# Performance work log

Measured on AMD Instinct MI355X. Metric: run time of the kernel, lower is better.

Reference implementation:

```python
import jax, jax.numpy as jnp
import numpy as np

HEADS = 16
DIM_HEAD = 64
EPS = 1e-8


def setup_inputs() -> dict:
    key = jax.random.key(0)
    ks = jax.random.split(key, 5)
    B, N, D = 2, 2048, 1024
    inner = HEADS * DIM_HEAD
    return {
        "x": jax.random.normal(ks[0], (B, N, D), jnp.float32),
        "Wq": jax.random.normal(ks[1], (D, inner), jnp.float32) * (D ** -0.5),
        "Wkv": jax.random.normal(ks[2], (D, 2 * inner), jnp.float32) * (D ** -0.5),
        "Wo": jax.random.normal(ks[3], (inner, D), jnp.float32) * (inner ** -0.5),
        "bo": jax.random.normal(ks[4], (D,), jnp.float32) * 0.02,
    }


def reference(x, Wq, Wkv, Wo, bo):
    # Self-attention (context = x), causal, memory-efficient path.
    # The chunked online-softmax in the source is mathematically equivalent to:
    #   gm = rowwise max of raw (unmasked) scores (stop-gradient, as in .detach())
    #   p  = exp(s - gm) with causal-masked entries zeroed (exp(-finfo.max) == 0)
    #   out = (p @ v) / (sum_j p + eps)
    B, N, D = x.shape
    H, Dh = HEADS, DIM_HEAD
    scale = Dh ** -0.5

    q = (x @ Wq).reshape(B, N, H, Dh).transpose(0, 2, 1, 3)  # b h n d
    kv = x @ Wkv
    k = kv[..., : H * Dh].reshape(B, N, H, Dh).transpose(0, 2, 1, 3)
    v = kv[..., H * Dh :].reshape(B, N, H, Dh).transpose(0, 2, 1, 3)

    s = jnp.einsum("bhid,bhjd->bhij", q * scale, k)  # b h i j
    gm = jax.lax.stop_gradient(jnp.max(s, axis=-1, keepdims=True))
    causal_mask = jnp.triu(jnp.ones((N, N), bool), 1)  # True above diagonal -> masked
    p = jnp.where(causal_mask, 0.0, jnp.exp(s - gm))
    num = jnp.einsum("bhij,bhjd->bhid", p, v)
    out = num / (jnp.sum(p, axis=-1, keepdims=True) + EPS)  # b h n d

    out = out.transpose(0, 2, 1, 3).reshape(B, N, H * Dh)  # b n (h d)
    return out @ Wo + bo
```

## Files before the change

### kernel.cpp

```cpp
#include <hip/hip_runtime.h>

typedef _Float16 f16;
typedef __attribute__((ext_vector_type(8))) _Float16 f16x8;
typedef __attribute__((ext_vector_type(4))) _Float16 f16x4;
typedef __attribute__((ext_vector_type(4))) float   f32x4;

typedef unsigned int u32;
typedef __attribute__((address_space(1))) const u32 gu32;
typedef __attribute__((address_space(3))) u32 lu32;

__device__ inline void gll16(const void* g, void* l) {
  __builtin_amdgcn_global_load_lds((gu32*)g, (lu32*)l, 16, 0, 0);
}

__global__ void prep(const float* __restrict__ Wq, const float* __restrict__ Wkv,
                     const float* __restrict__ Wo, const float* __restrict__ x,
                     f16* __restrict__ WqkvT, f16* __restrict__ WoT, f16* __restrict__ xb) {
  __shared__ float tile[32][33];
  int z = blockIdx.z;
  int tx = threadIdx.x, ty = threadIdx.y;
  if (z == 3) {
    size_t flat = ((size_t)(blockIdx.y * 64 + blockIdx.x) * 256 + ty * 32 + tx) * 2;
    for (int i = 0; i < 2; i++) {
      float4 v = ((const float4*)x)[flat + i];
      f16x4 r = { (f16)v.x, (f16)v.y, (f16)v.z, (f16)v.w };
      ((f16x4*)xb)[flat + i] = r;
    }
    return;
  }
  const float* src; f16* dst; int W;
  if (z == 0)      { src = Wq;  dst = WqkvT;                       W = 1024; }
  else if (z == 1) { src = Wkv; dst = WqkvT + (size_t)1024 * 1024; W = 2048; }
  else             { src = Wo;  dst = WoT;                         W = 1024; }
  int c0 = blockIdx.x * 32, r0 = blockIdx.y * 32;
  if (c0 >= W) return;
  for (int i = 0; i < 4; i++)
    tile[ty + i * 8][tx] = src[(size_t)(r0 + ty + i * 8) * W + c0 + tx];
  __syncthreads();
  for (int i = 0; i < 4; i++)
    dst[(size_t)(c0 + ty + i * 8) * 1024 + r0 + tx] = (f16)tile[tx][ty + i * 8];
}

__global__ __launch_bounds__(256) void gemm1(
    const f16* __restrict__ A, const f16* __restrict__ Bt,
    f16* __restrict__ qb, f16* __restrict__ kb, f16* __restrict__ vtb) {
  const int K = 1024;
  __shared__ f16 As[2][128 * 32];
  __shared__ f16 Bs[2][128 * 32];
  int tid = threadIdx.x;
  int wave = tid >> 6, lane = tid & 63, quad = lane >> 4, l16 = lane & 15;
  int m0 = blockIdx.y * 128, n0 = blockIdx.x * 128;
  int wr = (wave >> 1) * 64, wc = (wave & 1) * 64;

  f32x4 acc[4][4] = {};

  int gA = (((lane & 3) ^ ((lane >> 3) & 3))) * 8;
  const f16* Ag = A  + (size_t)(m0 + wave * 32 + (lane >> 2)) * K + gA;
  const f16* Bg = Bt + (size_t)(n0 + wave * 32 + (lane >> 2)) * K + gA;
  int rsz = (l16 >> 1) & 3;

  {
    f16* Asw = &As[0][0] + wave * 1024;
    f16* Bsw = &Bs[0][0] + wave * 1024;
    gll16(Ag, Asw);
    gll16(Ag + (size_t)16 * K, Asw + 512);
    gll16(Bg, Bsw);
    gll16(Bg + (size_t)16 * K, Bsw + 512);
  }
  __syncthreads();

  int cur = 0;
  for (int k0 = 0; k0 < K; k0 += 32) {
    if (k0 + 32 < K) {
      f16* Asw = &As[cur ^ 1][0] + wave * 1024;
      f16* Bsw = &Bs[cur ^ 1][0] + wave * 1024;
      gll16(Ag + k0 + 32, Asw);
      gll16(Ag + (size_t)16 * K + k0 + 32, Asw + 512);
      gll16(Bg + k0 + 32, Bsw);
      gll16(Bg + (size_t)16 * K + k0 + 32, Bsw + 512);
    }
    const f16* Asr = &As[cur][0];
    const f16* Bsr = &Bs[cur][0];
    f16x8 af[4], bf[4];
    for (int mt = 0; mt < 4; mt++)
      af[mt] = *(const f16x8*)&Asr[(wr + mt * 16 + l16) * 32 + ((quad ^ rsz) << 3)];
    for (int nt = 0; nt < 4; nt++)
      bf[nt] = *(const f16x8*)&Bsr[(wc + nt * 16 + l16) * 32 + ((quad ^ rsz) << 3)];
    for (int mt = 0; mt < 4; mt++)
      for (int nt = 0; nt < 4; nt++)
        acc[mt][nt] = __builtin_amdgcn_mfma_f32_16x16x32_f16(af[mt], bf[nt], acc[mt][nt], 0, 0, 0);
    __syncthreads();
    cur ^= 1;
  }

  if (n0 < 2048) {
    for (int mt = 0; mt < 4; mt++)
      for (int nt = 0; nt < 4; nt++)
        for (int r = 0; r < 4; r++) {
          int row = m0 + wr + mt * 16 + quad * 4 + r;
          int col = n0 + wc + nt * 16 + l16;
          float v = acc[mt][nt][r];
          int b = row >> 11, n = row & 2047;
          if (col < 1024) {
            qb[(((size_t)b * 16 + (col >> 6)) * 2048 + n) * 64 + (col & 63)] =
                (f16)(v * 0.1803368801111137f);
          } else {
            int c = col - 1024;
            kb[(((size_t)b * 16 + (c >> 6)) * 2048 + n) * 64 + (c & 63)] = (f16)v;
          }
        }
  } else {
    for (int mt = 0; mt < 4; mt++)
      for (int nt = 0; nt < 4; nt++) {
        int rb = m0 + wr + mt * 16 + quad * 4;
        int c  = n0 + wc + nt * 16 + l16 - 2048;
        int b = rb >> 11, n = rb & 2047;
        f16x4 pk = { (f16)acc[mt][nt][0], (f16)acc[mt][nt][1],
                     (f16)acc[mt][nt][2], (f16)acc[mt][nt][3] };
        size_t idx = (((size_t)(b * 16 + (c >> 6)) * 32 + (n >> 6)) * 64 + (c & 63)) * 64 + (n & 63);
        *(f16x4*)&vtb[idx] = pk;
      }
  }
}

__global__ __launch_bounds__(256) void gemm2(
    const f16* __restrict__ A, const f16* __restrict__ Bt,
    const float* __restrict__ bo, float* __restrict__ outf) {
  const int K = 1024;
  __shared__ f16 As[2][128 * 32];
  __shared__ f16 Bs[2][64 * 32];
  int tid = threadIdx.x;
  int wave = tid >> 6, lane = tid & 63, quad = lane >> 4, l16 = lane & 15;
  int m0 = blockIdx.y * 128, n0 = blockIdx.x * 64;
  int wr = (wave >> 1) * 64, wc = (wave & 1) * 32;

  f32x4 acc[4][2] = {};

  int gA = (((lane & 3) ^ ((lane >> 3) & 3))) * 8;
  const f16* Ag = A  + (size_t)(m0 + wave * 32 + (lane >> 2)) * K + gA;
  const f16* Bg = Bt + (size_t)(n0 + wave * 16 + (lane >> 2)) * K + gA;
  int rsz = (l16 >> 1) & 3;

  {
    f16* Asw = &As[0][0] + wave * 1024;
    f16* Bsw = &Bs[0][0] + wave * 512;
    gll16(Ag, Asw);
    gll16(Ag + (size_t)16 * K, Asw + 512);
    gll16(Bg, Bsw);
  }
  __syncthreads();

  int cur = 0;
  for (int k0 = 0; k0 < K; k0 += 32) {
    if (k0 + 32 < K) {
      f16* Asw = &As[cur ^ 1][0] + wave * 1024;
      f16* Bsw = &Bs[cur ^ 1][0] + wave * 512;
      gll16(Ag + k0 + 32, Asw);
      gll16(Ag + (size_t)16 * K + k0 + 32, Asw + 512);
      gll16(Bg + k0 + 32, Bsw);
    }
    const f16* Asr = &As[cur][0];
    const f16* Bsr = &Bs[cur][0];
    f16x8 af[4], bf[2];
    for (int mt = 0; mt < 4; mt++)
      af[mt] = *(const f16x8*)&Asr[(wr + mt * 16 + l16) * 32 + ((quad ^ rsz) << 3)];
    for (int nt = 0; nt < 2; nt++)
      bf[nt] = *(const f16x8*)&Bsr[(wc + nt * 16 + l16) * 32 + ((quad ^ rsz) << 3)];
    for (int mt = 0; mt < 4; mt++)
      for (int nt = 0; nt < 2; nt++)
        acc[mt][nt] = __builtin_amdgcn_mfma_f32_16x16x32_f16(af[mt], bf[nt], acc[mt][nt], 0, 0, 0);
    __syncthreads();
    cur ^= 1;
  }

  for (int mt = 0; mt < 4; mt++)
    for (int nt = 0; nt < 2; nt++)
      for (int r = 0; r < 4; r++) {
        int row = m0 + wr + mt * 16 + quad * 4 + r;
        int col = n0 + wc + nt * 16 + l16;
        outf[(size_t)row * 1024 + col] = acc[mt][nt][r] + bo[col];
      }
}

__global__ __launch_bounds__(256, 4) void attn(
    const f16* __restrict__ qb, const f16* __restrict__ kb,
    const f16* __restrict__ vtb, f16* __restrict__ ob) {
  __shared__ f16 Ks[2][64 * 64];
  __shared__ f16 Vs[2][64 * 64];
  __shared__ f16 Ps[4][16 * 64];
  int tid = threadIdx.x, wave = tid >> 6, lane = tid & 63, quad = lane >> 4, l16 = lane & 15;
  int l7 = l16 & 7;

  int bx = blockIdx.x;
  int q = bx >> 8, r = bx & 255;
  int xcd = r & 7, idx = r >> 3;
  int bh = xcd * 4 + (idx & 3);
  int srem = idx >> 2;
  int t = (q == 0) ? srem : (q == 1) ? 15 - srem : (q == 2) ? 16 + srem : 31 - srem;
  int qi0 = t * 64;
  int b = bh >> 4, h = bh & 15;

  const f16* Q  = qb + (size_t)bh * 2048 * 64;
  const char* Kg = (const char*)(kb + (size_t)bh * 2048 * 64);
  const char* Vbase = (const char*)(vtb + (size_t)bh * 32 * 4096);
  int wq0 = qi0 + wave * 16;
  int i = wq0 + l16;

  f16x8 qf[2];
  for (int ks = 0; ks < 2; ks++)
    qf[ks] = *(const f16x8*)&Q[(size_t)(wq0 + l16) * 64 + ks * 32 + quad * 8];

  f32x4 acc[4] = {};
  float lrow = 0.f;

  int sg = ((lane & 7) ^ ((lane >> 3) & 7)) * 16;
  int jl = wave * 16 + (lane >> 3);

  int end = qi0 + 64;

  gll16(Kg + (size_t)jl * 128 + sg,          (char*)&Ks[0][0] + wave * 2048);
  gll16(Kg + (size_t)(jl + 8) * 128 + sg,    (char*)&Ks[0][0] + wave * 2048 + 1024);
  gll16(Vbase + (size_t)jl * 128 + sg,       (char*)&Vs[0][0] + wave * 2048);
  gll16(Vbase + (size_t)(jl + 8) * 128 + sg, (char*)&Vs[0][0] + wave * 2048 + 1024);
  __syncthreads();

  int cur = 0;
  for (int j0 = 0; j0 < end; j0 += 64) {
    if (j0 + 64 < end) {
      const char* kg = Kg + (size_t)(j0 + 64) * 128;
      const char* vt = Vbase + (size_t)((j0 + 64) >> 6) * 8192;
      char* kd = (char*)&Ks[cur ^ 1][0] + wave * 2048;
      char* vd = (char*)&Vs[cur ^ 1][0] + wave * 2048;
      gll16(kg + (size_t)jl * 128 + sg,       kd);
      gll16(kg + (size_t)(jl + 8) * 128 + sg, kd + 1024);
      gll16(vt + (size_t)jl * 128 + sg,       vd);
      gll16(vt + (size_t)(jl + 8) * 128 + sg, vd + 1024);
    }

    {
      const f16* KsC = &Ks[cur][0];
      const f16* VsC = &Vs[cur][0];
      f16x8 kf[4][2], vf[4][2];
      for (int nt = 0; nt < 4; nt++)
        for (int ks = 0; ks < 2; ks++) {
          int pos = ((ks * 4 + quad) ^ l7) << 3;
          kf[nt][ks] = *(const f16x8*)&KsC[(nt * 16 + l16) * 64 + pos];
          vf[nt][ks] = *(const f16x8*)&VsC[(nt * 16 + l16) * 64 + pos];
        }

      f32x4 st[4];
      for (int nt = 0; nt < 4; nt++) {
        f32x4 z = {0.f, 0.f, 0.f, 0.f};
        z = __builtin_amdgcn_mfma_f32_16x16x32_f16(kf[nt][0], qf[0], z, 0, 0, 0);
        z = __builtin_amdgcn_mfma_f32_16x16x32_f16(kf[nt][1], qf[1], z, 0, 0, 0);
        st[nt] = z;
      }
      if (j0 + 63 > wq0) {
        for (int nt = 0; nt < 4; nt++) {
          int jc = j0 + nt * 16 + quad * 4;
          for (int rr = 0; rr < 4; rr++)
            st[nt][rr] = (jc + rr <= i) ? st[nt][rr] : -1e30f;
        }
      }
      float psum = 0.f;
      for (int nt = 0; nt < 4; nt++) {
        f16x4 pk;
        for (int rr = 0; rr < 4; rr++) {
          float p = __builtin_amdgcn_exp2f(st[nt][rr] - 14.426950408889634f);
          psum += p;
          pk[rr] = (f16)p;
        }
        int pos = (nt * 2 + (quad >> 1)) ^ l7;
        *(f16x4*)((char*)&Ps[wave][0] + l16 * 128 + pos * 16 + (quad & 1) * 8) = pk;
      }
      psum += __shfl_xor(psum, 16);
      psum += __shfl_xor(psum, 32);
      lrow += psum;

      for (int ks = 0; ks < 2; ks++) {
        f16x8 pf = *(const f16x8*)((char*)&Ps[wave][0] + l16 * 128 + (((ks * 4 + quad) ^ l7) * 16));
        for (int nt = 0; nt < 4; nt++)
          acc[nt] = __builtin_amdgcn_mfma_f32_16x16x32_f16(vf[nt][ks], pf, acc[nt], 0, 0, 0);
      }
    }
    __syncthreads();
    cur ^= 1;
  }

  float inv = 1.f / (lrow + 1e-8f);
  int n = wq0 + l16;
  for (int nt = 0; nt < 4; nt++) {
    f16x4 o = { (f16)(acc[nt][0] * inv), (f16)(acc[nt][1] * inv),
                (f16)(acc[nt][2] * inv), (f16)(acc[nt][3] * inv) };
    *(f16x4*)&ob[((size_t)b * 2048 + n) * 1024 + h * 64 + nt * 16 + quad * 4] = o;
  }
}

extern "C" void kernel_launch(void* const* d_in, const int* in_sizes, int n_in,
                              void* d_out, int out_size, void* d_ws, size_t ws_size,
                              hipStream_t stream) {
  const float* x   = (const float*)d_in[0];
  const float* Wq  = (const float*)d_in[1];
  const float* Wkv = (const float*)d_in[2];
  const float* Wo  = (const float*)d_in[3];
  const float* bo  = (const float*)d_in[4];
  float* out = (float*)d_out;

  char* ws = (char*)d_ws;
  f16* xb    = (f16*)ws;  ws += (size_t)4096 * 1024 * 2;
  f16* WqkvT = (f16*)ws;  ws += (size_t)3072 * 1024 * 2;
  f16* WoT   = (f16*)ws;  ws += (size_t)1024 * 1024 * 2;
  f16* qb    = (f16*)ws;  ws += (size_t)32 * 2048 * 64 * 2;
  f16* kb    = (f16*)ws;  ws += (size_t)32 * 2048 * 64 * 2;
  f16* vtb   = (f16*)ws;  ws += (size_t)32 * 64 * 2048 * 2;
  f16* ob    = xb;

  prep<<<dim3(64, 32, 4), dim3(32, 8), 0, stream>>>(Wq, Wkv, Wo, x, WqkvT, WoT, xb);
  gemm1<<<dim3(24, 32), 256, 0, stream>>>(xb, WqkvT, qb, kb, vtb);
  attn<<<dim3(1024), 256, 0, stream>>>(qb, kb, vtb, ob);
  gemm2<<<dim3(16, 32), 256, 0, stream>>>(ob, WoT, bo, out);
}
```

Before: 178.9 us.

## Restructure QKV GEMM into 256x256 tiles with 8 waves and phased MFMA scheduling

Rewrites the QKV projection GEMM to use 256x256 block tiles with 512 threads, K-tiles of 64 with XOR-swizzled LDS, and a two-buffer prefetch issued two tiles ahead. Each K-tile is split into four barrier-separated phases, with s_setprio raised around the MFMA bursts to interleave waves. The aim is more data reuse per LDS byte and better overlap of global loads with matrix math. The cost is that the grid shrinks to 192 blocks, which may underfill the 256 CUs, and that register pressure rises with 32 accumulators per thread.

```diff
diff --git a/kernel.cpp b/kernel.cpp
--- a/kernel.cpp
+++ b/kernel.cpp
@@ -41,60 +41,87 @@
     dst[(size_t)(c0 + ty + i * 8) * 1024 + r0 + tx] = (f16)tile[tx][ty + i * 8];
 }
 
-__global__ __launch_bounds__(256) void gemm1(
+#define G1_PHASE(qq, SA, SB, FIRST)                                          \
+  {                                                                          \
+    if (FIRST) {                                                             \
+      _Pragma("unroll") for (int nt = 0; nt < 4; nt++)                       \
+        _Pragma("unroll") for (int ks = 0; ks < 2; ks++)                     \
+          bf[nt][ks] = *(const f16x8*)&SB[(wc + nt * 16 + l16) * 64 +        \
+                                          (((ks * 4 + quad) ^ l7) << 3)];    \
+    }                                                                        \
+    _Pragma("unroll") for (int j = 0; j < 2; j++)                            \
+      _Pragma("unroll") for (int ks = 0; ks < 2; ks++)                       \
+        af[j][ks] = *(const f16x8*)&SA[(wr + (2 * (qq) + j) * 16 + l16) * 64 \
+                                       + (((ks * 4 + quad) ^ l7) << 3)];     \
+    __builtin_amdgcn_s_barrier();                                            \
+    asm volatile("s_waitcnt lgkmcnt(0)" ::: "memory");                       \
+    __builtin_amdgcn_s_setprio(1);                                           \
+    _Pragma("unroll") for (int j = 0; j < 2; j++)                            \
+      _Pragma("unroll") for (int nt = 0; nt < 4; nt++) {                     \
+        acc[2 * (qq) + j][nt] = __builtin_amdgcn_mfma_f32_16x16x32_f16(      \
+            af[j][0], bf[nt][0], acc[2 * (qq) + j][nt], 0, 0, 0);            \
+        acc[2 * (qq) + j][nt] = __builtin_amdgcn_mfma_f32_16x16x32_f16(      \
+            af[j][1], bf[nt][1], acc[2 * (qq) + j][nt], 0, 0, 0);            \
+      }                                                                      \
+    __builtin_amdgcn_s_setprio(0);                                           \
+  }
+
+#define G1_STAGE(ktile, SA, SB)                                              \
+  { int kk = (ktile) * 64;                                                   \
+    _Pragma("unroll") for (int i2 = 0; i2 < 4; i2++) {                       \
+      gll16(Ag0 + (size_t)(i2 * 64) * 1024 + kk,                             \
+            (char*)(SA) + i2 * 8192 + wave * 1024);                          \
+      gll16(Bg0 + (size_t)(i2 * 64) * 1024 + kk,                             \
+            (char*)(SB) + i2 * 8192 + wave * 1024);                          \
+    } }
+
+#define G1_TILE(ktv, SA, SB)                                                 \
+  G1_PHASE(0, SA, SB, 1) __builtin_amdgcn_s_barrier();                       \
+  G1_PHASE(1, SA, SB, 0) __builtin_amdgcn_s_barrier();                       \
+  G1_PHASE(2, SA, SB, 0) __builtin_amdgcn_s_barrier();                       \
+  G1_PHASE(3, SA, SB, 0)                                                     \
+  if ((ktv) < 14) {                                                          \
+    G1_STAGE((ktv) + 2, SA, SB)                                              \
+    asm volatile("s_waitcnt vmcnt(8)" ::: "memory");                         \
+  } else if ((ktv) == 14) {                                                  \
+    asm volatile("s_waitcnt vmcnt(0)" ::: "memory");                         \
+  }                                                                          \
+  if ((ktv) < 15) __builtin_amdgcn_s_barrier();
+
+__global__ __launch_bounds__(512) void gemm1(
     const f16* __restrict__ A, const f16* __restrict__ Bt,
     f16* __restrict__ qb, f16* __restrict__ kb, f16* __restrict__ vtb) {
-  const int K = 1024;
-  __shared__ f16 As[2][128 * 32];
-  __shared__ f16 Bs[2][128 * 32];
+  __shared__ f16 As0[256 * 64];
+  __shared__ f16 Bs0[256 * 64];
+  __shared__ f16 As1[256 * 64];
+  __shared__ f16 Bs1[256 * 64];
   int tid = threadIdx.x;
-  int wave = tid >> 6, lane = tid & 63, quad = lane >> 4, l16 = lane & 15;
-  int m0 = blockIdx.y * 128, n0 = blockIdx.x * 128;
-  int wr = (wave >> 1) * 64, wc = (wave & 1) * 64;
-
-  f32x4 acc[4][4] = {};
-
-  int gA = (((lane & 3) ^ ((lane >> 3) & 3))) * 8;
-  const f16* Ag = A  + (size_t)(m0 + wave * 32 + (lane >> 2)) * K + gA;
-  const f16* Bg = Bt + (size_t)(n0 + wave * 32 + (lane >> 2)) * K + gA;
-  int rsz = (l16 >> 1) & 3;
-
-  {
-    f16* Asw = &As[0][0] + wave * 1024;
-    f16* Bsw = &Bs[0][0] + wave * 1024;
-    gll16(Ag, Asw);
-    gll16(Ag + (size_t)16 * K, Asw + 512);
-    gll16(Bg, Bsw);
-    gll16(Bg + (size_t)16 * K, Bsw + 512);
-  }
-  __syncthreads();
-
-  int cur = 0;
-  for (int k0 = 0; k0 < K; k0 += 32) {
-    if (k0 + 32 < K) {
-      f16* Asw = &As[cur ^ 1][0] + wave * 1024;
-      f16* Bsw = &Bs[cur ^ 1][0] + wave * 1024;
-      gll16(Ag + k0 + 32, Asw);
-      gll16(Ag + (size_t)16 * K + k0 + 32, Asw + 512);
-      gll16(Bg + k0 + 32, Bsw);
-      gll16(Bg + (size_t)16 * K + k0 + 32, Bsw + 512);
-    }
-    const f16* Asr = &As[cur][0];
-    const f16* Bsr = &Bs[cur][0];
-    f16x8 af[4], bf[4];
-    for (int mt = 0; mt < 4; mt++)
-      af[mt] = *(const f16x8*)&Asr[(wr + mt * 16 + l16) * 32 + ((quad ^ rsz) << 3)];
-    for (int nt = 0; nt < 4; nt++)
-      bf[nt] = *(const f16x8*)&Bsr[(wc + nt * 16 + l16) * 32 + ((quad ^ rsz) << 3)];
-    for (int mt = 0; mt < 4; mt++)
-      for (int nt = 0; nt < 4; nt++)
-        acc[mt][nt] = __builtin_amdgcn_mfma_f32_16x16x32_f16(af[mt], bf[nt], acc[mt][nt], 0, 0, 0);
-    __syncthreads();
-    cur ^= 1;
+  int wave = tid >> 6, lane = tid & 63, quad = (lane >> 4) & 3, l16 = lane & 15;
+  int l7 = l16 & 7;
+  int m0 = blockIdx.y * 256, n0 = blockIdx.x * 256;
+  int wr = (wave >> 2) * 128, wc = (wave & 3) * 64;
+
+  f32x4 acc[8][4] = {};
+  f16x8 af[2][2], bf[4][2];
+
+  int jl8 = tid >> 3;
+  int sgc = ((tid & 7) ^ ((tid >> 3) & 7)) * 8;
+  const f16* Ag0 = A  + (size_t)(m0 + jl8) * 1024 + sgc;
+  const f16* Bg0 = Bt + (size_t)(n0 + jl8) * 1024 + sgc;
+
+  G1_STAGE(0, As0, Bs0)
+  G1_STAGE(1, As1, Bs1)
+  asm volatile("s_waitcnt vmcnt(8)" ::: "memory");
+  __builtin_amdgcn_s_barrier();
+
+#pragma unroll 1
+  for (int kt = 0; kt < 16; kt += 2) {
+    G1_TILE(kt,     As0, Bs0)
+    G1_TILE(kt + 1, As1, Bs1)
   }
 
   if (n0 < 2048) {
-    for (int mt = 0; mt < 4; mt++)
+    for (int mt = 0; mt < 8; mt++)
       for (int nt = 0; nt < 4; nt++)
         for (int r = 0; r < 4; r++) {
           int row = m0 + wr + mt * 16 + quad * 4 + r;
@@ -110,7 +137,7 @@
           }
         }
   } else {
-    for (int mt = 0; mt < 4; mt++)
+    for (int mt = 0; mt < 8; mt++)
       for (int nt = 0; nt < 4; nt++) {
         int rb = m0 + wr + mt * 16 + quad * 4;
         int c  = n0 + wc + nt * 16 + l16 - 2048;
@@ -316,7 +343,7 @@
   f16* ob    = xb;
 
   prep<<<dim3(64, 32, 4), dim3(32, 8), 0, stream>>>(Wq, Wkv, Wo, x, WqkvT, WoT, xb);
-  gemm1<<<dim3(24, 32), 256, 0, stream>>>(xb, WqkvT, qb, kb, vtb);
+  gemm1<<<dim3(12, 16), 512, 0, stream>>>(xb, WqkvT, qb, kb, vtb);
   attn<<<dim3(1024), 256, 0, stream>>>(qb, kb, vtb, ob);
   gemm2<<<dim3(16, 32), 256, 0, stream>>>(ob, WoT, bo, out);
 }
```

Result: no change. 181.3 us (+1.4%).
